# Performance work log

Measured on AMD Instinct MI355X. Metric: run time of the kernel, lower is better.

## Reference

```python
import jax, jax.numpy as jnp
from jax import lax
import numpy as np


def _conv(x, w, b, stride=1, pad=1):
    y = lax.conv_general_dilated(x, w, (stride, stride), ((pad, pad), (pad, pad)),
                                 dimension_numbers=('NCHW', 'OIHW', 'NCHW'))
    return y + b[None, :, None, None]


def _deconv(x, w, b):
    # PyTorch ConvTranspose2d(k=3, s=2, p=1, output_padding=1); w is torch layout (Cin, Cout, 3, 3)
    wt = jnp.flip(w, (2, 3)).transpose(1, 0, 2, 3)  # (Cout, Cin, 3, 3)
    y = lax.conv_general_dilated(x, wt, (1, 1), ((1, 2), (1, 2)), lhs_dilation=(2, 2),
                                 dimension_numbers=('NCHW', 'OIHW', 'NCHW'))
    return y + b[None, :, None, None]


def _lrelu(x):
    return jnp.where(x >= 0, x, 0.01 * x)


def _nonlocal(x, tw, tb, pw, pb, gw, gb, ww, wb):
    # embedded-Gaussian non-local block with residual (NONLocalBlock2D)
    B, C, H, W = x.shape
    N = H * W
    th = _conv(x, tw, tb, 1, 0).reshape(B, -1, N)
    ph = _conv(x, pw, pb, 1, 0).reshape(B, -1, N)
    g = _conv(x, gw, gb, 1, 0).reshape(B, -1, N)
    attn = jax.nn.softmax(jnp.einsum('bcn,bcm->bnm', th, ph), axis=-1)  # [B,N,N]
    y = jnp.einsum('bnm,bcm->bcn', attn, g).reshape(B, -1, H, W)
    return _conv(y, ww, wb, 1, 0) + x


def _deform_conv(x, offset, mask, w, b):
    # modulated deformable conv (DCNv2-style), k=3 s=1 p=1, zero padding outside bounds
    B, C, H, W = x.shape
    K2 = 9
    ky, kx = jnp.meshgrid(jnp.arange(3) - 1, jnp.arange(3) - 1, indexing='ij')
    ky = ky.reshape(-1).astype(x.dtype)
    kx = kx.reshape(-1).astype(x.dtype)
    off = offset.reshape(B, K2, 2, H, W)  # (dy, dx) interleaved per kernel tap
    py = jnp.arange(H, dtype=x.dtype)[None, None, :, None] + ky[None, :, None, None] + off[:, :, 0]
    px = jnp.arange(W, dtype=x.dtype)[None, None, None, :] + kx[None, :, None, None] + off[:, :, 1]
    y0 = jnp.floor(py)
    x0 = jnp.floor(px)
    wy1 = py - y0
    wx1 = px - x0
    xf = x.reshape(B, C, H * W)

    def gather(yi, xi):
        valid = ((yi >= 0) & (yi < H) & (xi >= 0) & (xi < W)).astype(x.dtype)
        yc = jnp.clip(yi, 0, H - 1).astype(jnp.int32)
        xc = jnp.clip(xi, 0, W - 1).astype(jnp.int32)
        idx = (yc * W + xc).reshape(B, 1, K2 * H * W)
        v = jnp.take_along_axis(xf, idx, axis=2).reshape(B, C, K2, H, W)
        return v * valid[:, None]

    val = (gather(y0, x0) * ((1 - wy1) * (1 - wx1))[:, None]
           + gather(y0, x0 + 1) * ((1 - wy1) * wx1)[:, None]
           + gather(y0 + 1, x0) * (wy1 * (1 - wx1))[:, None]
           + gather(y0 + 1, x0 + 1) * (wy1 * wx1)[:, None])
    val = val * mask[:, None]  # modulation
    return jnp.einsum('bckhw,ock->bohw', val, w.reshape(w.shape[0], C, K2)) + b[None, :, None, None]


def _forward(x_all, ms_fine, ms_coarse, enc_w0, enc_b0, enc_w1, enc_b1,
             nl0_tw, nl0_tb, nl0_pw, nl0_pb, nl0_gw, nl0_gb, nl0_ww, nl0_wb,
             nl1_tw, nl1_tb, nl1_pw, nl1_pb, nl1_gw, nl1_gb, nl1_ww, nl1_wb,
             dec_w0, dec_b0, dec_w1, dec_b1, off_w, off_b, dcn_w, dcn_b):
    def motion(pc, cc, pf, cf):
        # scale 0 (coarse, reversed order), mot_mode='concat'
        e0 = _lrelu(_conv(jnp.concatenate([pc, cc], 1), enc_w0, enc_b0, 2, 1))
        m0 = e0 + _nonlocal(e0, nl0_tw, nl0_tb, nl0_pw, nl0_pb, nl0_gw, nl0_gb, nl0_ww, nl0_wb)
        u0 = _lrelu(_deconv(m0, dec_w0, dec_b0))
        # scale 1 (fine)
        e1 = _lrelu(_conv(jnp.concatenate([pf, cf], 1), enc_w1, enc_b1, 2, 1))
        m1 = e1 + _nonlocal(e1, nl1_tw, nl1_tb, nl1_pw, nl1_pb, nl1_gw, nl1_gb, nl1_ww, nl1_wb)
        return _lrelu(_deconv(m1 + u0, dec_w1, dec_b1))

    aligned = [x_all[0]]
    for s in range(1, x_all.shape[0]):  # seq_len - 1 alignments
        mot = motion(ms_coarse[s], ms_coarse[0], ms_fine[s], ms_fine[0])
        est = _conv(mot, off_w, off_b, 1, 1)  # [B, 27, H, W]
        offset = est[:, 9:]
        mask = jax.nn.sigmoid(est[:, :9])
        aligned.append(_deform_conv(x_all[s], offset, mask, dcn_w, dcn_b))
    return jnp.stack(aligned)


def setup_inputs() -> dict:
    key = jax.random.key(0)
    ks = iter(jax.random.split(key, 48))

    def rn(shape, scale=1.0):
        return jax.random.normal(next(ks), shape, dtype=jnp.float32) * scale

    S, B = 3, 2
    inp = {
        'x_all': rn((S, B, 128, 128, 128)),
        'ms_fine': rn((S, B, 128, 128, 128)),
        'ms_coarse': rn((S, B, 256, 64, 64)),
        'enc_w0': rn((64, 512, 3, 3), 0.02), 'enc_b0': rn((64,), 0.02),
        'enc_w1': rn((64, 256, 3, 3), 0.02), 'enc_b1': rn((64,), 0.02),
    }
    for i in range(2):
        inp[f'nl{i}_tw'] = rn((32, 64, 1, 1), 0.05); inp[f'nl{i}_tb'] = rn((32,), 0.02)
        inp[f'nl{i}_pw'] = rn((32, 64, 1, 1), 0.05); inp[f'nl{i}_pb'] = rn((32,), 0.02)
        inp[f'nl{i}_gw'] = rn((32, 64, 1, 1), 0.05); inp[f'nl{i}_gb'] = rn((32,), 0.02)
        inp[f'nl{i}_ww'] = rn((64, 32, 1, 1), 0.05); inp[f'nl{i}_wb'] = rn((64,), 0.02)
    inp['dec_w0'] = rn((64, 64, 3, 3), 0.05); inp['dec_b0'] = rn((64,), 0.02)
    inp['dec_w1'] = rn((64, 64, 3, 3), 0.05); inp['dec_b1'] = rn((64,), 0.02)
    inp['off_w'] = rn((27, 64, 3, 3), 0.02); inp['off_b'] = rn((27,), 0.02)
    inp['dcn_w'] = rn((128, 128, 3, 3), 0.03); inp['dcn_b'] = rn((128,), 0.02)
    return inp


def reference(x_all, ms_fine, ms_coarse, enc_w0, enc_b0, enc_w1, enc_b1,
              nl0_tw, nl0_tb, nl0_pw, nl0_pb, nl0_gw, nl0_gb, nl0_ww, nl0_wb,
              nl1_tw, nl1_tb, nl1_pw, nl1_pb, nl1_gw, nl1_gb, nl1_ww, nl1_wb,
              dec_w0, dec_b0, dec_w1, dec_b1, off_w, off_b, dcn_w, dcn_b):
    return _forward(x_all, ms_fine, ms_coarse, enc_w0, enc_b0, enc_w1, enc_b1,
                    nl0_tw, nl0_tb, nl0_pw, nl0_pb, nl0_gw, nl0_gb, nl0_ww, nl0_wb,
                    nl1_tw, nl1_tb, nl1_pw, nl1_pb, nl1_gw, nl1_gb, nl1_ww, nl1_wb,
                    dec_w0, dec_b0, dec_w1, dec_b1, off_w, off_b, dcn_w, dcn_b)
```

## Files before the change

### kernel.cpp

```cpp
#include <hip/hip_runtime.h>
#include <math.h>

typedef __attribute__((ext_vector_type(8))) short bf16x8;
typedef __attribute__((ext_vector_type(4))) float f32x4;
typedef unsigned short ushort_t;
typedef unsigned int uint_t;

__device__ __forceinline__ float lrelu_f(float x) { return x >= 0.f ? x : 0.01f * x; }

__device__ __forceinline__ ushort_t f2bf(float f) {
    uint_t x = __float_as_uint(f);
    uint_t r = (x + 0x7fffu + ((x >> 16) & 1u)) >> 16;
    return (ushort_t)r;
}

__device__ __forceinline__ uint_t pack_bf16(float lo, float hi) {
    uint_t out;
    asm("v_cvt_pk_bf16_f32 %0, %1, %2" : "=v"(out) : "v"(lo), "v"(hi));
    return out;
}

__device__ __forceinline__ float fexp2(float x) {
    float r;
    asm("v_exp_f32 %0, %1" : "=v"(r) : "v"(x));
    return r;
}

__global__ __launch_bounds__(256) void castw2_kernel(const float* __restrict__ w,
    ushort_t* __restrict__ w2, int Cout, int Cin, int K, int deconv)
{
    int idx = blockIdx.x * 256 + threadIdx.x;
    if (idx >= 64 * K) return;
    int co = idx / K, kp = idx % K;
    int cb = kp / 288;
    int r  = kp % 288;
    int tap = r >> 5, cl = r & 31;
    int ci = cb * 32 + cl;
    float val = 0.f;
    if (co < Cout)
        val = deconv ? w[(size_t)(ci * Cout + co) * 9 + (8 - tap)]
                     : w[(size_t)(co * Cin + ci) * 9 + tap];
    w2[idx] = f2bf(val);
}

template<int STRIDE, int MODE>
__global__ __launch_bounds__(256) void conv3x3_mfma(
    const float* __restrict__ inA, const float* __restrict__ inB, int CinA,
    size_t sStrideA, int Hin, int Win, int Cin,
    const ushort_t* __restrict__ w2, int K,
    int Wout, int Npx, int tilesPerMap, int ksplit, int chunksPerKs,
    float* __restrict__ part,
    const float* __restrict__ bias, int act, int CoutStore, float* __restrict__ outDirect)
{
    __shared__ ushort_t sB[64 * 40];
    int tile = blockIdx.x % tilesPerMap;
    int ks   = (blockIdx.x / tilesPerMap) % ksplit;
    int b4   = blockIdx.x / (tilesPerMap * ksplit);
    int s_idx = b4 >> 1, bb = b4 & 1;
    int tid  = threadIdx.x;
    int wave = tid >> 6, lane = tid & 63;
    int lrow = lane & 15, lkg = lane >> 4;
    int px  = tid & 63;
    int cio = wave * 8;
    int p   = tile * 64 + px;
    int oy  = p / Wout, ox = p - oy * Wout;
    int HWin = Hin * Win;
    int CinB = Cin - CinA;

    f32x4 acc[4];
    #pragma unroll
    for (int n2 = 0; n2 < 4; ++n2) acc[n2] = (f32x4){0.f, 0.f, 0.f, 0.f};

    for (int cch = 0; cch < chunksPerKs; ++cch) {
        int chunkIdx = ks * chunksPerKs + cch;
        int cb  = chunkIdx / 9;
        int tap = chunkIdx - cb * 9;
        int cib = cb * 32;
        int ky = tap / 3, kx = tap - ky * 3;
        float msk;
        int offp;
        if (MODE == 0) {
            int iy = oy * STRIDE - 1 + ky;
            int ix = ox * STRIDE - 1 + kx;
            bool vld = (iy >= 0) && (iy < Hin) && (ix >= 0) && (ix < Win);
            msk = vld ? 1.f : 0.f;
            offp = min(max(iy, 0), Hin - 1) * Win + min(max(ix, 0), Win - 1);
        } else {
            int uy = oy + ky, ux = ox + kx;
            int r = (uy - 1) >> 1, q = (ux - 1) >> 1;
            bool vld = (uy & 1) && (ux & 1) && (r < Hin) && (q < Win);
            msk = vld ? 1.f : 0.f;
            offp = min(max(r, 0), Hin - 1) * Win + min(max(q, 0), Win - 1);
        }
        int c = cib + cio;
        const float* src = (c < CinA)
            ? inA + s_idx * sStrideA + (size_t)(bb * CinA + c) * HWin
            : inB + (size_t)(bb * CinB + (c - CinA)) * HWin;
        float v[8];
        #pragma unroll
        for (int j = 0; j < 8; ++j) v[j] = src[(size_t)j * HWin + offp] * msk;
        uint4 pk;
        pk.x = pack_bf16(v[0], v[1]);
        pk.y = pack_bf16(v[2], v[3]);
        pk.z = pack_bf16(v[4], v[5]);
        pk.w = pack_bf16(v[6], v[7]);
        __syncthreads();
        *(uint4*)&sB[px * 40 + cio] = pk;
        __syncthreads();

        const ushort_t* wr = w2 + (size_t)(wave * 16 + lrow) * K + chunkIdx * 32 + lkg * 8;
        bf16x8 afr = *(const bf16x8*)wr;
        #pragma unroll
        for (int n2 = 0; n2 < 4; ++n2) {
            bf16x8 bfr = *(const bf16x8*)&sB[(n2 * 16 + lrow) * 40 + lkg * 8];
            acc[n2] = __builtin_amdgcn_mfma_f32_16x16x32_bf16(afr, bfr, acc[n2], 0, 0, 0);
        }
    }

    if (bias) {
        #pragma unroll
        for (int n2 = 0; n2 < 4; ++n2) {
            #pragma unroll
            for (int j = 0; j < 4; ++j) {
                int co = wave * 16 + lkg * 4 + j;
                if (co < CoutStore) {
                    int pp = tile * 64 + n2 * 16 + lrow;
                    float r = acc[n2][j] + bias[co];
                    if (act) r = lrelu_f(r);
                    outDirect[((size_t)(b4 * CoutStore + co)) * (size_t)Npx + pp] = r;
                }
            }
        }
    } else {
        #pragma unroll
        for (int n2 = 0; n2 < 4; ++n2) {
            #pragma unroll
            for (int j = 0; j < 4; ++j) {
                int co = wave * 16 + lkg * 4 + j;
                int pp = tile * 64 + n2 * 16 + lrow;
                part[((size_t)(ks * 4 + b4) * 64 + co) * (size_t)Npx + pp] = acc[n2][j];
            }
        }
    }
}

__global__ __launch_bounds__(256) void reduce_bias_act(const float* __restrict__ part,
    const float* __restrict__ bias, float* __restrict__ out,
    int Cout, int Npx, int ksplit, int act)
{
    int idx = blockIdx.x * 256 + threadIdx.x;
    int total = 4 * Cout * Npx;
    if (idx >= total) return;
    int p  = idx % Npx;
    int co = (idx / Npx) % Cout;
    int b4 = idx / (Npx * Cout);
    float s = bias[co];
    for (int ks = 0; ks < ksplit; ++ks)
        s += part[(((size_t)ks * 4 + b4) * 64 + co) * (size_t)Npx + p];
    if (act) s = lrelu_f(s);
    out[((size_t)b4 * Cout + co) * (size_t)Npx + p] = s;
}

__global__ __launch_bounds__(256) void castw_perm_kernel(const float* __restrict__ w,
    ushort_t* __restrict__ wbf)
{
    int idx = blockIdx.x * 256 + threadIdx.x;
    if (idx >= 147456) return;
    int co = idx / 1152;
    int r  = idx % 1152;
    int chunk = r / 288;
    int r2 = r % 288;
    int tap = r2 >> 5;
    int cl  = r2 & 31;
    int ci = chunk * 32 + cl;
    wbf[idx] = f2bf(w[(size_t)co * 1152 + ci * 9 + tap]);
}

__global__ __launch_bounds__(256) void transpose_nhwc_bf16(const float* __restrict__ x,
    ushort_t* __restrict__ xT)
{
    __shared__ float t[32][33];
    int cT = blockIdx.x & 3;
    int pT = (blockIdx.x >> 2) & 511;
    int b4 = blockIdx.x >> 11;
    int tx = threadIdx.x & 31, ty = threadIdx.x >> 5;
    const float* src = x + ((size_t)((b4 + 2) * 128) + cT * 32) * 16384 + (size_t)pT * 32;
    #pragma unroll
    for (int i = 0; i < 4; ++i)
        t[ty + 8 * i][tx] = src[(size_t)(ty + 8 * i) * 16384 + tx];
    __syncthreads();
    ushort_t* dst = xT + ((size_t)b4 * 16384 + (size_t)pT * 32) * 128 + cT * 32;
    #pragma unroll
    for (int i = 0; i < 4; ++i)
        dst[(size_t)(ty + 8 * i) * 128 + tx] = f2bf(t[tx][ty + 8 * i]);
}

__global__ __launch_bounds__(256) void conv1x1x3_bf16(const float* __restrict__ e, int N,
    const float* __restrict__ tw, const float* __restrict__ tb,
    const float* __restrict__ pw, const float* __restrict__ pb,
    const float* __restrict__ gw, const float* __restrict__ gb,
    ushort_t* __restrict__ thT, ushort_t* __restrict__ phT, ushort_t* __restrict__ gT)
{
    __shared__ float sw[32 * 64];
    __shared__ float sb[32];
    int tid = threadIdx.x;
    int idx = blockIdx.x * 256 + tid;
    int j = idx / (4 * N);
    const float* wsel = (j == 0) ? tw : (j == 1) ? pw : gw;
    const float* bsel = (j == 0) ? tb : (j == 1) ? pb : gb;
    for (int i = tid; i < 2048; i += 256) sw[i] = wsel[i];
    if (tid < 32) sb[tid] = bsel[tid];
    __syncthreads();
    int rem = idx - j * 4 * N;
    int n = rem % N, b4 = rem / N;
    float ein[64];
    const float* ep = e + (size_t)b4 * 64 * N + n;
    #pragma unroll
    for (int ci = 0; ci < 64; ++ci) ein[ci] = ep[(size_t)ci * N];

    float val[32];
    #pragma unroll
    for (int cc = 0; cc < 32; ++cc) {
        float acc = sb[cc];
        const float* wr = &sw[cc * 64];
        #pragma unroll
        for (int ci = 0; ci < 64; ++ci) acc = fmaf(wr[ci], ein[ci], acc);
        val[cc] = acc;
    }
    if (j == 0) {
        #pragma unroll
        for (int cc = 0; cc < 32; ++cc) val[cc] *= 1.44269504f;
    }
    if (j < 2) {
        ushort_t* row = (j == 0 ? thT : phT) + ((size_t)b4 * N + n) * 32;
        #pragma unroll
        for (int w4 = 0; w4 < 4; ++w4) {
            uint4 pk;
            pk.x = pack_bf16(val[8 * w4 + 0], val[8 * w4 + 1]);
            pk.y = pack_bf16(val[8 * w4 + 2], val[8 * w4 + 3]);
            pk.z = pack_bf16(val[8 * w4 + 4], val[8 * w4 + 5]);
            pk.w = pack_bf16(val[8 * w4 + 6], val[8 * w4 + 7]);
            *(uint4*)(row + 8 * w4) = pk;
        }
    } else {
        #pragma unroll
        for (int cc = 0; cc < 32; ++cc)
            gT[((size_t)b4 * 32 + cc) * N + n] = f2bf(val[cc]);
    }
}

__global__ __launch_bounds__(256) void attn_flash(const ushort_t* __restrict__ thT,
    const ushort_t* __restrict__ phT, const ushort_t* __restrict__ gT,
    float* __restrict__ partO, float* __restrict__ partML, int N, int KVS)
{
    __shared__ ushort_t sP[4][16 * 40];
    int tid  = threadIdx.x;
    int wave = tid >> 6, lane = tid & 63;
    int lq = lane & 15, lkg = lane >> 4;
    int nqb = N / 64;
    int ks = blockIdx.x % KVS;
    int qb = (blockIdx.x / KVS) % nqb;
    int b4 = blockIdx.x / (KVS * nqb);
    int q0w = qb * 64 + wave * 16;
    int chunk = N / KVS;
    int m_start = ks * chunk;

    bf16x8 qf = *(const bf16x8*)(thT + ((size_t)b4 * N + q0w + lq) * 32 + 8 * lkg);

    float m_run = -1e30f, l_run = 0.f;
    f32x4 acc[2];
    acc[0] = (f32x4){0.f, 0.f, 0.f, 0.f};
    acc[1] = (f32x4){0.f, 0.f, 0.f, 0.f};

    for (int m0 = m_start; m0 < m_start + chunk; m0 += 64) {
        f32x4 tf[4];
        #pragma unroll
        for (int f = 0; f < 4; ++f) {
            bf16x8 kf = *(const bf16x8*)(phT + ((size_t)b4 * N + m0 + f * 16 + lq) * 32 + 8 * lkg);
            tf[f] = __builtin_amdgcn_mfma_f32_16x16x32_bf16(kf, qf,
                        (f32x4){0.f, 0.f, 0.f, 0.f}, 0, 0, 0);
        }

        float mx = -1e30f;
        #pragma unroll
        for (int f = 0; f < 4; ++f)
            #pragma unroll
            for (int r = 0; r < 4; ++r) mx = fmaxf(mx, tf[f][r]);
        mx = fmaxf(mx, __shfl_xor(mx, 16));
        mx = fmaxf(mx, __shfl_xor(mx, 32));

        if (__any(mx > m_run)) {
            float m_new = fmaxf(m_run, mx);
            float scale = fexp2(m_run - m_new);
            l_run *= scale;
            m_run = m_new;
            float sc[4];
            #pragma unroll
            for (int r = 0; r < 4; ++r) sc[r] = __shfl(scale, 4 * lkg + r);
            #pragma unroll
            for (int h = 0; h < 2; ++h)
                #pragma unroll
                for (int r = 0; r < 4; ++r) acc[h][r] *= sc[r];
        }

        float rs = 0.f;
        #pragma unroll
        for (int f = 0; f < 4; ++f)
            #pragma unroll
            for (int r = 0; r < 4; ++r) {
                float pv = fexp2(tf[f][r] - m_run);
                tf[f][r] = pv;
                rs += pv;
            }
        rs += __shfl_xor(rs, 16);
        rs += __shfl_xor(rs, 32);
        l_run += rs;

        #pragma unroll
        for (int f = 0; f < 4; ++f) {
            *(uint_t*)&sP[wave][lq * 40 + f * 16 + 4 * lkg]     = pack_bf16(tf[f][0], tf[f][1]);
            *(uint_t*)&sP[wave][lq * 40 + f * 16 + 4 * lkg + 2] = pack_bf16(tf[f][2], tf[f][3]);
        }

        #pragma unroll
        for (int mc = 0; mc < 2; ++mc) {
            bf16x8 pf = *(const bf16x8*)&sP[wave][lq * 40 + mc * 32 + 8 * lkg];
            #pragma unroll
            for (int h = 0; h < 2; ++h) {
                bf16x8 vf = *(const bf16x8*)(gT + ((size_t)b4 * 32 + h * 16 + lq) * N
                                             + m0 + mc * 32 + 8 * lkg);
                acc[h] = __builtin_amdgcn_mfma_f32_16x16x32_bf16(pf, vf, acc[h], 0, 0, 0);
            }
        }
    }

    #pragma unroll
    for (int h = 0; h < 2; ++h) {
        #pragma unroll
        for (int r = 0; r < 4; ++r) {
            int q = q0w + 4 * lkg + r;
            partO[(((size_t)ks * 4 + b4) * N + q) * 32 + h * 16 + lq] = acc[h][r];
        }
    }
    if (lane < 16) {
        size_t mlo = (((size_t)ks * 4 + b4) * N + q0w + lq) * 2;
        partML[mlo]     = m_run;
        partML[mlo + 1] = l_run;
    }
}

__global__ __launch_bounds__(256) void nl_merge_fused(const float* __restrict__ e,
    const float* __restrict__ partO, const float* __restrict__ partML,
    const float* __restrict__ u,
    const float* __restrict__ ww, const float* __restrict__ wb,
    float* __restrict__ out, int N, int KVS)
{
    __shared__ float sw[64 * 32];
    __shared__ float sb[64];
    int tid = threadIdx.x;
    for (int i = tid; i < 2048; i += 256) sw[i] = ww[i];
    if (tid < 64) sb[tid] = wb[tid];
    __syncthreads();
    int idx = blockIdx.x * 256 + tid;
    int n = idx % N;
    int cog = (idx / N) & 3;
    int b4 = idx / (4 * N);

    float mstar = -1e30f;
    for (int ks = 0; ks < KVS; ++ks)
        mstar = fmaxf(mstar, partML[(((size_t)ks * 4 + b4) * N + n) * 2]);
    float denom = 0.f;
    float yv[32];
    #pragma unroll
    for (int c = 0; c < 32; ++c) yv[c] = 0.f;
    for (int ks = 0; ks < KVS; ++ks) {
        size_t mlo = (((size_t)ks * 4 + b4) * N + n) * 2;
        float w = fexp2(partML[mlo] - mstar);
        denom += w * partML[mlo + 1];
        const f32x4* op = (const f32x4*)(partO + (((size_t)ks * 4 + b4) * N + n) * 32);
        #pragma unroll
        for (int jj = 0; jj < 8; ++jj) {
            f32x4 v = op[jj];
            #pragma unroll
            for (int t = 0; t < 4; ++t) yv[4 * jj + t] = fmaf(w, v[t], yv[4 * jj + t]);
        }
    }
    float inv = 1.f / denom;
    #pragma unroll
    for (int i = 0; i < 16; ++i) {
        int co = cog * 16 + i;
        float dot = 0.f;
        const float* wr = &sw[co * 32];
        #pragma unroll
        for (int c = 0; c < 32; ++c) dot = fmaf(wr[c], yv[c], dot);
        size_t o = (size_t)b4 * 64 * N + (size_t)co * N + n;
        float r = sb[co] + inv * dot + 2.f * e[o];
        if (u) r += u[o];
        out[o] = r;
    }
}

__global__ __launch_bounds__(512, 6) void deform_mfma6(const ushort_t* __restrict__ xT,
    const float* __restrict__ est, const ushort_t* __restrict__ wbf,
    const float* __restrict__ bias, float* __restrict__ out)
{
    const int H = 128, W = 128, HW = 16384;
    const int BS = 296;
    __shared__ ushort_t sB[64 * BS];
    __shared__ float4 sW[576];
    __shared__ uint2  sO[576];
    int id  = blockIdx.x;
    int lin = (id & 7) * 128 + (id >> 3);
    int tile = lin & 255;
    int b4   = lin >> 8;
    int p0   = tile * 64;
    int tid  = threadIdx.x;

    const float* eb = est + (size_t)b4 * 27 * HW;
    for (int i = tid; i < 576; i += 512) {
        int k = i >> 6, j = i & 63;
        int p = p0 + j;
        int yy = p >> 7, xx = p & 127;
        float oy = eb[(size_t)(9 + 2 * k) * HW + p];
        float ox = eb[(size_t)(10 + 2 * k) * HW + p];
        float mv = eb[(size_t)k * HW + p];
        float mk = 1.f / (1.f + __expf(-mv));
        float py = (float)(yy + (k / 3) - 1) + oy;
        float qx = (float)(xx + (k % 3) - 1) + ox;
        float fy0 = floorf(py), fx0 = floorf(qx);
        float wy = py - fy0, wx = qx - fx0;
        int y0 = (int)fy0, x0 = (int)fx0;
        int y1 = y0 + 1, x1 = x0 + 1;
        bool yv0 = (y0 >= 0) && (y0 < H), yv1 = (y1 >= 0) && (y1 < H);
        bool xv0 = (x0 >= 0) && (x0 < W), xv1 = (x1 >= 0) && (x1 < W);
        int y0c = min(max(y0, 0), H - 1), y1c = min(max(y1, 0), H - 1);
        int x0c = min(max(x0, 0), W - 1), x1c = min(max(x1, 0), W - 1);
        float4 w4;
        w4.x = (yv0 && xv0) ? (1.f - wy) * (1.f - wx) * mk : 0.f;
        w4.y = (yv0 && xv1) ? (1.f - wy) * wx * mk : 0.f;
        w4.z = (yv1 && xv0) ? wy * (1.f - wx) * mk : 0.f;
        w4.w = (yv1 && xv1) ? wy * wx * mk : 0.f;
        sW[i] = w4;
        uint_t o00 = (uint_t)(y0c * W + x0c), o01 = (uint_t)(y0c * W + x1c);
        uint_t o10 = (uint_t)(y1c * W + x0c), o11 = (uint_t)(y1c * W + x1c);
        sO[i] = (uint2){ o00 | (o01 << 16), o10 | (o11 << 16) };
    }

    int wave = tid >> 6, lane = tid & 63;
    int co_base = wave * 16;
    int lrow = lane & 15, lkg = lane >> 4;
    int cg = tid & 3;

    f32x4 acc[4];
    #pragma unroll
    for (int n2 = 0; n2 < 4; ++n2) acc[n2] = (f32x4){0.f, 0.f, 0.f, 0.f};

    const ushort_t* xb = xT + (size_t)b4 * HW * 128;

    for (int cc = 0; cc < 128; cc += 32) {
        __syncthreads();
        #pragma unroll
        for (int it = 0; it < 5; ++it) {
            int task = it * 512 + tid;
            if (task < 2304) {
                int si = task >> 2;
                float4 w4 = sW[si];
                uint2 o4 = sO[si];
                int chb = cc + cg * 8;
                uint4 u00 = *(const uint4*)(xb + (size_t)(o4.x & 0xFFFFu) * 128 + chb);
                uint4 u01 = *(const uint4*)(xb + (size_t)(o4.x >> 16) * 128 + chb);
                uint4 u10 = *(const uint4*)(xb + (size_t)(o4.y & 0xFFFFu) * 128 + chb);
                uint4 u11 = *(const uint4*)(xb + (size_t)(o4.y >> 16) * 128 + chb);
                float v[8];
                const uint_t* a0 = (const uint_t*)&u00;
                const uint_t* a1 = (const uint_t*)&u01;
                const uint_t* a2 = (const uint_t*)&u10;
                const uint_t* a3 = (const uint_t*)&u11;
                #pragma unroll
                for (int q = 0; q < 4; ++q) {
                    float c00l = __uint_as_float(a0[q] << 16), c00h = __uint_as_float(a0[q] & 0xffff0000u);
                    float c01l = __uint_as_float(a1[q] << 16), c01h = __uint_as_float(a1[q] & 0xffff0000u);
                    float c10l = __uint_as_float(a2[q] << 16), c10h = __uint_as_float(a2[q] & 0xffff0000u);
                    float c11l = __uint_as_float(a3[q] << 16), c11h = __uint_as_float(a3[q] & 0xffff0000u);
                    v[2 * q]     = w4.x * c00l + w4.y * c01l + w4.z * c10l + w4.w * c11l;
                    v[2 * q + 1] = w4.x * c00h + w4.y * c01h + w4.z * c10h + w4.w * c11h;
                }
                int pxl = si & 63, tap = si >> 6;
                uint4 pk;
                pk.x = pack_bf16(v[0], v[1]);
                pk.y = pack_bf16(v[2], v[3]);
                pk.z = pack_bf16(v[4], v[5]);
                pk.w = pack_bf16(v[6], v[7]);
                *(uint4*)&sB[pxl * BS + tap * 32 + cg * 8] = pk;
            }
        }
        __syncthreads();
        int kbase = cc * 9;
        #pragma unroll
        for (int ks = 0; ks < 9; ++ks) {
            bf16x8 afr = *reinterpret_cast<const bf16x8*>(
                wbf + (size_t)(co_base + lrow) * 1152 + kbase + ks * 32 + lkg * 8);
            #pragma unroll
            for (int n2 = 0; n2 < 4; ++n2) {
                bf16x8 bfr = *reinterpret_cast<const bf16x8*>(
                    &sB[(n2 * 16 + lrow) * BS + ks * 32 + lkg * 8]);
                acc[n2] = __builtin_amdgcn_mfma_f32_16x16x32_bf16(afr, bfr, acc[n2], 0, 0, 0);
            }
        }
    }

    #pragma unroll
    for (int j = 0; j < 4; ++j) {
        int co = co_base + lkg * 4 + j;
        float bb = bias[co];
        #pragma unroll
        for (int n2 = 0; n2 < 4; ++n2) {
            int px = p0 + n2 * 16 + lrow;
            out[((size_t)((b4 + 2) * 128 + co)) * HW + px] = acc[n2][j] + bb;
        }
    }
}

extern "C" void kernel_launch(void* const* d_in, const int* in_sizes, int n_in,
                              void* d_out, int out_size, void* d_ws, size_t ws_size,
                              hipStream_t stream)
{
    const float* x_all     = (const float*)d_in[0];
    const float* ms_fine   = (const float*)d_in[1];
    const float* ms_coarse = (const float*)d_in[2];
    const float* enc_w0 = (const float*)d_in[3];
    const float* enc_b0 = (const float*)d_in[4];
    const float* enc_w1 = (const float*)d_in[5];
    const float* enc_b1 = (const float*)d_in[6];
    const float* nl_tw[2] = { (const float*)d_in[7],  (const float*)d_in[15] };
    const float* nl_tb[2] = { (const float*)d_in[8],  (const float*)d_in[16] };
    const float* nl_pw[2] = { (const float*)d_in[9],  (const float*)d_in[17] };
    const float* nl_pb[2] = { (const float*)d_in[10], (const float*)d_in[18] };
    const float* nl_gw[2] = { (const float*)d_in[11], (const float*)d_in[19] };
    const float* nl_gb[2] = { (const float*)d_in[12], (const float*)d_in[20] };
    const float* nl_ww[2] = { (const float*)d_in[13], (const float*)d_in[21] };
    const float* nl_wb[2] = { (const float*)d_in[14], (const float*)d_in[22] };
    const float* dec_w0 = (const float*)d_in[23];
    const float* dec_b0 = (const float*)d_in[24];
    const float* dec_w1 = (const float*)d_in[25];
    const float* dec_b1 = (const float*)d_in[26];
    const float* off_w  = (const float*)d_in[27];
    const float* off_b  = (const float*)d_in[28];
    const float* dcn_w  = (const float*)d_in[29];
    const float* dcn_b  = (const float*)d_in[30];

    float* ws = (float*)d_ws;
    ushort_t* wbf     = (ushort_t*)ws;
    ushort_t* w2_enc0 = wbf + 147456;
    ushort_t* w2_enc1 = w2_enc0 + 294912;
    ushort_t* w2_dec0 = w2_enc1 + 147456;
    ushort_t* w2_dec1 = w2_dec0 + 36864;
    ushort_t* w2_est  = w2_dec1 + 36864;
    float* U1      = ws + 350208;
    float* u0      = U1 + 1048576;
    float* e1      = u0 + 1048576;
    float* partML  = e1 + 1048576;
    float* regPart = partML + 262144;
    float* regMot  = regPart + 2097152;

    float* e0 = U1;
    ushort_t* thT0 = (ushort_t*)(U1 + 262144);
    ushort_t* phT0 = thT0 + 131072;
    ushort_t* gT0  = phT0 + 131072;
    float* m0 = U1 + 458752;
    ushort_t* thT1 = (ushort_t*)U1;
    ushort_t* phT1 = thT1 + 524288;
    ushort_t* gT1  = phT1 + 524288;
    float* m1  = U1;
    float* mot = regMot;
    ushort_t* xTb = (ushort_t*)regMot;
    float* est = regPart;
    float* partO1 = regMot;

    float* out = (float*)d_out;
    const size_t frame  = (size_t)2 * 128 * 128 * 128;
    const size_t cframe = (size_t)2 * 256 * 64 * 64;

    hipMemcpyAsync(out, x_all, frame * sizeof(float), hipMemcpyDeviceToDevice, stream);

    castw_perm_kernel<<<(147456 + 255) / 256, 256, 0, stream>>>(dcn_w, wbf);
    castw2_kernel<<<(64 * 4608 + 255) / 256, 256, 0, stream>>>(enc_w0, w2_enc0, 64, 512, 4608, 0);
    castw2_kernel<<<(64 * 2304 + 255) / 256, 256, 0, stream>>>(enc_w1, w2_enc1, 64, 256, 2304, 0);
    castw2_kernel<<<(64 * 576 + 255) / 256, 256, 0, stream>>>(dec_w0, w2_dec0, 64, 64, 576, 1);
    castw2_kernel<<<(64 * 576 + 255) / 256, 256, 0, stream>>>(dec_w1, w2_dec1, 64, 64, 576, 1);
    castw2_kernel<<<(64 * 576 + 255) / 256, 256, 0, stream>>>(off_w, w2_est, 27, 64, 576, 0);


    conv3x3_mfma<2, 0><<<4 * 16 * 8, 256, 0, stream>>>(
        ms_coarse + cframe, ms_coarse, 256, cframe, 64, 64, 512,
        w2_enc0, 4608, 32, 1024, 16, 8, 18, regPart, nullptr, 0, 0, nullptr);
    reduce_bias_act<<<1024, 256, 0, stream>>>(regPart, enc_b0, e0, 64, 1024, 8, 1);

    conv1x1x3_bf16<<<48, 256, 0, stream>>>(e0, 1024,
        nl_tw[0], nl_tb[0], nl_pw[0], nl_pb[0], nl_gw[0], nl_gb[0], thT0, phT0, gT0);
    attn_flash<<<4 * 16 * 8, 256, 0, stream>>>(thT0, phT0, gT0, regPart, partML, 1024, 8);
    nl_merge_fused<<<64, 256, 0, stream>>>(e0, regPart, partML, nullptr,
        nl_ww[0], nl_wb[0], m0, 1024, 8);

    conv3x3_mfma<1, 1><<<4 * 64 * 2, 256, 0, stream>>>(
        m0, m0, 64, (size_t)2 * 64 * 1024, 32, 32, 64,
        w2_dec0, 576, 64, 4096, 64, 2, 9, regPart, nullptr, 0, 0, nullptr);
    reduce_bias_act<<<4096, 256, 0, stream>>>(regPart, dec_b0, u0, 64, 4096, 2, 1);

    conv3x3_mfma<2, 0><<<4 * 64 * 2, 256, 0, stream>>>(
        ms_fine + frame, ms_fine, 128, frame, 128, 128, 256,
        w2_enc1, 2304, 64, 4096, 64, 2, 36, regPart, nullptr, 0, 0, nullptr);
    reduce_bias_act<<<4096, 256, 0, stream>>>(regPart, enc_b1, e1, 64, 4096, 2, 1);

    conv1x1x3_bf16<<<192, 256, 0, stream>>>(e1, 4096,
        nl_tw[1], nl_tb[1], nl_pw[1], nl_pb[1], nl_gw[1], nl_gb[1], thT1, phT1, gT1);
    attn_flash<<<4 * 64 * 8, 256, 0, stream>>>(thT1, phT1, gT1, partO1, partML, 4096, 8);
    nl_merge_fused<<<256, 256, 0, stream>>>(e1, partO1, partML, u0,
        nl_ww[1], nl_wb[1], m1, 4096, 8);

    conv3x3_mfma<1, 1><<<4 * 256, 256, 0, stream>>>(
        m1, m1, 64, (size_t)2 * 64 * 4096, 64, 64, 64,
        w2_dec1, 576, 128, 16384, 256, 1, 18, regPart, dec_b1, 1, 64, mot);

    conv3x3_mfma<1, 0><<<4 * 256, 256, 0, stream>>>(
        mot, mot, 64, (size_t)2 * 64 * 16384, 128, 128, 64,
        w2_est, 576, 128, 16384, 256, 1, 18, regPart, off_b, 0, 27, est);

    transpose_nhwc_bf16<<<8192, 256, 0, stream>>>(x_all, xTb);
    deform_mfma6<<<1024, 512, 0, stream>>>(xTb, est, wbf, dcn_b, out);
}
```

Before: 361.4 us.

## Keep deform sampling metadata in registers and gather 64 channels per pass

The deformable-conv kernel now computes bilinear weights and offsets straight into registers, each thread owning 9 sample slots, in place of staging them through shared memory. It gathers 64 channels per pass (two passes) instead of 32 (four passes), which halves the barrier-separated gather/MFMA phases and widens each thread's channel slice to 8 groups. The cost is a shared tile roughly twice as large and more registers per thread, so the occupancy hint is lowered from 6 to 4.

```diff
diff --git a/kernel.cpp b/kernel.cpp
--- a/kernel.cpp
+++ b/kernel.cpp
@@ -400,15 +400,13 @@
     }
 }
 
-__global__ __launch_bounds__(512, 6) void deform_mfma6(const ushort_t* __restrict__ xT,
+__global__ __launch_bounds__(512, 4) void deform_mfma7(const ushort_t* __restrict__ xT,
     const float* __restrict__ est, const ushort_t* __restrict__ wbf,
     const float* __restrict__ bias, float* __restrict__ out)
 {
     const int H = 128, W = 128, HW = 16384;
-    const int BS = 296;
+    const int BS = 584;
     __shared__ ushort_t sB[64 * BS];
-    __shared__ float4 sW[576];
-    __shared__ uint2  sO[576];
     int id  = blockIdx.x;
     int lin = (id & 7) * 128 + (id >> 3);
     int tile = lin & 255;
@@ -416,95 +414,105 @@
     int p0   = tile * 64;
     int tid  = threadIdx.x;
 
-    const float* eb = est + (size_t)b4 * 27 * HW;
-    for (int i = tid; i < 576; i += 512) {
-        int k = i >> 6, j = i & 63;
-        int p = p0 + j;
-        int yy = p >> 7, xx = p & 127;
-        float oy = eb[(size_t)(9 + 2 * k) * HW + p];
-        float ox = eb[(size_t)(10 + 2 * k) * HW + p];
-        float mv = eb[(size_t)k * HW + p];
-        float mk = 1.f / (1.f + __expf(-mv));
-        float py = (float)(yy + (k / 3) - 1) + oy;
-        float qx = (float)(xx + (k % 3) - 1) + ox;
-        float fy0 = floorf(py), fx0 = floorf(qx);
-        float wy = py - fy0, wx = qx - fx0;
-        int y0 = (int)fy0, x0 = (int)fx0;
-        int y1 = y0 + 1, x1 = x0 + 1;
-        bool yv0 = (y0 >= 0) && (y0 < H), yv1 = (y1 >= 0) && (y1 < H);
-        bool xv0 = (x0 >= 0) && (x0 < W), xv1 = (x1 >= 0) && (x1 < W);
-        int y0c = min(max(y0, 0), H - 1), y1c = min(max(y1, 0), H - 1);
-        int x0c = min(max(x0, 0), W - 1), x1c = min(max(x1, 0), W - 1);
-        float4 w4;
-        w4.x = (yv0 && xv0) ? (1.f - wy) * (1.f - wx) * mk : 0.f;
-        w4.y = (yv0 && xv1) ? (1.f - wy) * wx * mk : 0.f;
-        w4.z = (yv1 && xv0) ? wy * (1.f - wx) * mk : 0.f;
-        w4.w = (yv1 && xv1) ? wy * wx * mk : 0.f;
-        sW[i] = w4;
-        uint_t o00 = (uint_t)(y0c * W + x0c), o01 = (uint_t)(y0c * W + x1c);
-        uint_t o10 = (uint_t)(y1c * W + x0c), o11 = (uint_t)(y1c * W + x1c);
-        sO[i] = (uint2){ o00 | (o01 << 16), o10 | (o11 << 16) };
+    float4 rW[9];
+    uint2  rO[9];
+    {
+        const float* eb = est + (size_t)b4 * 27 * HW;
+        int s0 = tid >> 3;
+        #pragma unroll
+        for (int it = 0; it < 9; ++it) {
+            int si = it * 64 + s0;
+            int k = si >> 6, j = si & 63;
+            int p = p0 + j;
+            int yy = p >> 7, xx = p & 127;
+            float oy = eb[(size_t)(9 + 2 * k) * HW + p];
+            float ox = eb[(size_t)(10 + 2 * k) * HW + p];
+            float mv = eb[(size_t)k * HW + p];
+            float mk = 1.f / (1.f + __expf(-mv));
+            float py = (float)(yy + (k / 3) - 1) + oy;
+            float qx = (float)(xx + (k % 3) - 1) + ox;
+            float fy0 = floorf(py), fx0 = floorf(qx);
+            float wy = py - fy0, wx = qx - fx0;
+            int y0 = (int)fy0, x0 = (int)fx0;
+            int y1 = y0 + 1, x1 = x0 + 1;
+            bool yv0 = (y0 >= 0) && (y0 < H), yv1 = (y1 >= 0) && (y1 < H);
+            bool xv0 = (x0 >= 0) && (x0 < W), xv1 = (x1 >= 0) && (x1 < W);
+            int y0c = min(max(y0, 0), H - 1), y1c = min(max(y1, 0), H - 1);
+            int x0c = min(max(x0, 0), W - 1), x1c = min(max(x1, 0), W - 1);
+            float4 w4;
+            w4.x = (yv0 && xv0) ? (1.f - wy) * (1.f - wx) * mk : 0.f;
+            w4.y = (yv0 && xv1) ? (1.f - wy) * wx * mk : 0.f;
+            w4.z = (yv1 && xv0) ? wy * (1.f - wx) * mk : 0.f;
+            w4.w = (yv1 && xv1) ? wy * wx * mk : 0.f;
+            rW[it] = w4;
+            uint_t o00 = (uint_t)(y0c * W + x0c), o01 = (uint_t)(y0c * W + x1c);
+            uint_t o10 = (uint_t)(y1c * W + x0c), o11 = (uint_t)(y1c * W + x1c);
+            rO[it] = (uint2){ o00 | (o01 << 16), o10 | (o11 << 16) };
+        }
     }
 
     int wave = tid >> 6, lane = tid & 63;
     int co_base = wave * 16;
     int lrow = lane & 15, lkg = lane >> 4;
-    int cg = tid & 3;
+    int cg = tid & 7;
 
     f32x4 acc[4];
     #pragma unroll
     for (int n2 = 0; n2 < 4; ++n2) acc[n2] = (f32x4){0.f, 0.f, 0.f, 0.f};
 
     const ushort_t* xb = xT + (size_t)b4 * HW * 128;
-
-    for (int cc = 0; cc < 128; cc += 32) {
+    int colb = (cg >> 2) * 288 + (cg & 3) * 8;
+    int chb_local = cg * 8;
+
+    for (int pass = 0; pass < 2; ++pass) {
+        int chp = pass * 64 + chb_local;
         __syncthreads();
         #pragma unroll
-        for (int it = 0; it < 5; ++it) {
-            int task = it * 512 + tid;
-            if (task < 2304) {
-                int si = task >> 2;
-                float4 w4 = sW[si];
-                uint2 o4 = sO[si];
-                int chb = cc + cg * 8;
-                uint4 u00 = *(const uint4*)(xb + (size_t)(o4.x & 0xFFFFu) * 128 + chb);
-                uint4 u01 = *(const uint4*)(xb + (size_t)(o4.x >> 16) * 128 + chb);
-                uint4 u10 = *(const uint4*)(xb + (size_t)(o4.y & 0xFFFFu) * 128 + chb);
-                uint4 u11 = *(const uint4*)(xb + (size_t)(o4.y >> 16) * 128 + chb);
-                float v[8];
-                const uint_t* a0 = (const uint_t*)&u00;
-                const uint_t* a1 = (const uint_t*)&u01;
-                const uint_t* a2 = (const uint_t*)&u10;
-                const uint_t* a3 = (const uint_t*)&u11;
+        for (int it = 0; it < 9; ++it) {
+            int si = it * 64 + (tid >> 3);
+            float4 w4 = rW[it];
+            uint2 o4 = rO[it];
+            uint4 u00 = *(const uint4*)(xb + (size_t)(o4.x & 0xFFFFu) * 128 + chp);
+            uint4 u01 = *(const uint4*)(xb + (size_t)(o4.x >> 16) * 128 + chp);
+            uint4 u10 = *(const uint4*)(xb + (size_t)(o4.y & 0xFFFFu) * 128 + chp);
+            uint4 u11 = *(const uint4*)(xb + (size_t)(o4.y >> 16) * 128 + chp);
+            float v[8];
+            const uint_t* a0 = (const uint_t*)&u00;
+            const uint_t* a1 = (const uint_t*)&u01;
+            const uint_t* a2 = (const uint_t*)&u10;
+            const uint_t* a3 = (const uint_t*)&u11;
+            #pragma unroll
+            for (int q = 0; q < 4; ++q) {
+                float c00l = __uint_as_float(a0[q] << 16), c00h = __uint_as_float(a0[q] & 0xffff0000u);
+                float c01l = __uint_as_float(a1[q] << 16), c01h = __uint_as_float(a1[q] & 0xffff0000u);
+                float c10l = __uint_as_float(a2[q] << 16), c10h = __uint_as_float(a2[q] & 0xffff0000u);
+                float c11l = __uint_as_float(a3[q] << 16), c11h = __uint_as_float(a3[q] & 0xffff0000u);
+                v[2 * q]     = w4.x * c00l + w4.y * c01l + w4.z * c10l + w4.w * c11l;
+                v[2 * q + 1] = w4.x * c00h + w4.y * c01h + w4.z * c10h + w4.w * c11h;
+            }
+            int pxl = si & 63, tap = si >> 6;
+            uint4 pk;
+            pk.x = pack_bf16(v[0], v[1]);
+            pk.y = pack_bf16(v[2], v[3]);
+            pk.z = pack_bf16(v[4], v[5]);
+            pk.w = pack_bf16(v[6], v[7]);
+            *(uint4*)&sB[pxl * BS + colb + tap * 32] = pk;
+        }
+        __syncthreads();
+        #pragma unroll
+        for (int cbl = 0; cbl < 2; ++cbl) {
+            int kbase_w = (pass * 2 + cbl) * 288;
+            int kbase_s = cbl * 288;
+            #pragma unroll
+            for (int ks = 0; ks < 9; ++ks) {
+                bf16x8 afr = *reinterpret_cast<const bf16x8*>(
+                    wbf + (size_t)(co_base + lrow) * 1152 + kbase_w + ks * 32 + lkg * 8);
                 #pragma unroll
-                for (int q = 0; q < 4; ++q) {
-                    float c00l = __uint_as_float(a0[q] << 16), c00h = __uint_as_float(a0[q] & 0xffff0000u);
-                    float c01l = __uint_as_float(a1[q] << 16), c01h = __uint_as_float(a1[q] & 0xffff0000u);
-                    float c10l = __uint_as_float(a2[q] << 16), c10h = __uint_as_float(a2[q] & 0xffff0000u);
-                    float c11l = __uint_as_float(a3[q] << 16), c11h = __uint_as_float(a3[q] & 0xffff0000u);
-                    v[2 * q]     = w4.x * c00l + w4.y * c01l + w4.z * c10l + w4.w * c11l;
-                    v[2 * q + 1] = w4.x * c00h + w4.y * c01h + w4.z * c10h + w4.w * c11h;
+                for (int n2 = 0; n2 < 4; ++n2) {
+                    bf16x8 bfr = *reinterpret_cast<const bf16x8*>(
+                        &sB[(n2 * 16 + lrow) * BS + kbase_s + ks * 32 + lkg * 8]);
+                    acc[n2] = __builtin_amdgcn_mfma_f32_16x16x32_bf16(afr, bfr, acc[n2], 0, 0, 0);
                 }
-                int pxl = si & 63, tap = si >> 6;
-                uint4 pk;
-                pk.x = pack_bf16(v[0], v[1]);
-                pk.y = pack_bf16(v[2], v[3]);
-                pk.z = pack_bf16(v[4], v[5]);
-                pk.w = pack_bf16(v[6], v[7]);
-                *(uint4*)&sB[pxl * BS + tap * 32 + cg * 8] = pk;
-            }
-        }
-        __syncthreads();
-        int kbase = cc * 9;
-        #pragma unroll
-        for (int ks = 0; ks < 9; ++ks) {
-            bf16x8 afr = *reinterpret_cast<const bf16x8*>(
-                wbf + (size_t)(co_base + lrow) * 1152 + kbase + ks * 32 + lkg * 8);
-            #pragma unroll
-            for (int n2 = 0; n2 < 4; ++n2) {
-                bf16x8 bfr = *reinterpret_cast<const bf16x8*>(
-                    &sB[(n2 * 16 + lrow) * BS + ks * 32 + lkg * 8]);
-                acc[n2] = __builtin_amdgcn_mfma_f32_16x16x32_bf16(afr, bfr, acc[n2], 0, 0, 0);
             }
         }
     }
@@ -627,5 +635,5 @@
         w2_est, 576, 128, 16384, 256, 1, 18, regPart, off_b, 0, 27, est);
 
     transpose_nhwc_bf16<<<8192, 256, 0, stream>>>(x_all, xTb);
-    deform_mfma6<<<1024, 512, 0, stream>>>(xTb, est, wbf, dcn_b, out);
-}
+    deform_mfma7<<<1024, 512, 0, stream>>>(xTb, est, wbf, dcn_b, out);
+}
```

Measured after the change: 394.8 us. 1.09x slower.
